# Optimization experiments

Measured on AMD Instinct MI355X. Metric: run time of the kernel, lower is better.

Reference implementation:

```python
import jax, jax.numpy as jnp
import numpy as np

N = 100_000          # nodes
E = 1_600_000        # edges (avg degree 16)
LRELU = 0.01         # default nn.LeakyReLU slope (MLP / bottleneck)
SLOPE = 0.2          # GAT attention slope


def leaky(x, s):
    return jnp.where(x >= 0, x, s * x)


def dense_block(x, convW, gamma, beta):
    # x: [N, C0]; convW: [L, G, Cmax]; each layer: BN -> LeakyReLU -> 1x1 conv -> concat
    for i in range(convW.shape[0]):
        c = x.shape[1]                       # static under trace
        mu = x.mean(axis=0)
        var = x.var(axis=0)                  # biased var, matches torch BN train mode
        xn = (x - mu) * jax.lax.rsqrt(var + 1e-5) * gamma[i, :c] + beta[i, :c]
        xn = leaky(xn, LRELU)
        x = jnp.concatenate([x, xn @ convW[i, :, :c].T], axis=1)  # [N, c+G]
    return x


def gat(x, W, a, b, src, dst):
    # single effective head (torch code shares weight/a across heads -> identical heads)
    h = x @ W                                # [N, F]
    F = W.shape[1]
    # per-edge logit: LeakyReLU([h_dst || h_src] @ a)
    e = leaky(h[dst] @ a[:F] + h[src] @ a[F:], SLOPE)   # [E]
    m = jax.ops.segment_max(e, dst, num_segments=N)
    m = jnp.where(jnp.isfinite(m), m, 0.0)
    ex = jnp.exp(e - m[dst])
    den = jax.ops.segment_sum(ex, dst, num_segments=N)
    alpha = ex / (den[dst] + 1e-16)
    out = jax.ops.segment_sum(alpha[:, None] * h[src], dst, num_segments=N)
    return out + b


def setup_inputs() -> dict:
    key = jax.random.key(0)
    ks = jax.random.split(key, 16)

    def w(k, shape, fan_in):
        return jax.random.normal(k, shape, jnp.float32) / np.float32(np.sqrt(fan_in))

    return {
        "x": jax.random.normal(ks[0], (N, 64), jnp.float32),
        "src": jax.random.randint(ks[1], (E,), 0, N, jnp.int64 if jax.config.jax_enable_x64 else jnp.int32),
        "dst": jax.random.randint(ks[2], (E,), 0, N, jnp.int64 if jax.config.jax_enable_x64 else jnp.int32),
        "mlp_w1": w(ks[3], (64, 256), 64),
        "mlp_b1": jnp.zeros((256,), jnp.float32),
        "mlp_w2": w(ks[4], (256, 256), 256),
        "mlp_b2": jnp.zeros((256,), jnp.float32),
        "mlp_w3": w(ks[5], (256, 24), 256),
        "mlp_b3": jnp.zeros((24,), jnp.float32),
        "conv1": w(ks[6], (6, 12, 84), 84),
        "bn1_g": jnp.ones((6, 84), jnp.float32),
        "bn1_b": jnp.zeros((6, 84), jnp.float32),
        "gat1_w": w(ks[7], (96, 48), 96),
        "gat1_a": jax.random.normal(ks[8], (96,), jnp.float32) * 0.1,
        "gat1_b": jnp.zeros((48,), jnp.float32),
        "conv2": w(ks[9], (6, 12, 108), 108),
        "bn2_g": jnp.ones((6, 108), jnp.float32),
        "bn2_b": jnp.zeros((6, 108), jnp.float32),
        "gat2_w": w(ks[10], (120, 60), 120),
        "gat2_a": jax.random.normal(ks[11], (120,), jnp.float32) * 0.1,
        "gat2_b": jnp.zeros((60,), jnp.float32),
        "conv3": w(ks[12], (6, 12, 120), 120),
        "bn3_g": jnp.ones((6, 120), jnp.float32),
        "bn3_b": jnp.zeros((6, 120), jnp.float32),
    }


def reference(x, src, dst,
              mlp_w1, mlp_b1, mlp_w2, mlp_b2, mlp_w3, mlp_b3,
              conv1, bn1_g, bn1_b, gat1_w, gat1_a, gat1_b,
              conv2, bn2_g, bn2_b, gat2_w, gat2_a, gat2_b,
              conv3, bn3_g, bn3_b):
    h = leaky(x @ mlp_w1 + mlp_b1, LRELU)
    h = leaky(h @ mlp_w2 + mlp_b2, LRELU)
    h = leaky(h @ mlp_w3 + mlp_b3, LRELU)          # [N, 24]
    h = dense_block(h, conv1, bn1_g, bn1_b)        # [N, 96]
    h = gat(h, gat1_w, gat1_a, gat1_b, src, dst)   # [N, 48]
    h = dense_block(h, conv2, bn2_g, bn2_b)        # [N, 120]
    h = gat(h, gat2_w, gat2_a, gat2_b, src, dst)   # [N, 60]
    h = dense_block(h, conv3, bn3_g, bn3_b)        # [N, 132]
    return h
```

## Files before the change

kernel.cpp:

```cpp
#include <hip/hip_runtime.h>
#include <math.h>

#define N_NODES 100000
#define N_EDGES 1600000

static constexpr int GG = (N_NODES + 63) / 64;
static constexpr int NB = (N_NODES + 255) / 256;
static constexpr int NBKT = (N_NODES + 255) / 256;

typedef __attribute__((ext_vector_type(8))) short          bf16x8;
typedef __attribute__((ext_vector_type(8))) unsigned short ushort8_t;
typedef __attribute__((ext_vector_type(4))) unsigned short ushort4_t;
typedef __attribute__((ext_vector_type(4))) float          f32x4;

__device__ __forceinline__ float lrelu(float v, float s){ return v >= 0.f ? v : v*s; }

__device__ __forceinline__ unsigned short f2bf(float f){
    unsigned u = __float_as_uint(f);
    unsigned r = (u + 0x7FFFu + ((u >> 16) & 1u)) >> 16;
    return (unsigned short)r;
}
__device__ __forceinline__ float bf2f(unsigned short h){
    return __uint_as_float(((unsigned)h) << 16);
}

__global__ void cvt_wT_split(const float* __restrict__ w,
                             unsigned short* __restrict__ whi,
                             unsigned short* __restrict__ wlo,
                             int K, int Nsrc, int Npad)
{
    int idx = blockIdx.x * 256 + threadIdx.x;
    if (idx >= Npad * K) return;
    int n = idx / K, k = idx % K;
    float v = (n < Nsrc) ? w[(long)k * Nsrc + n] : 0.f;
    unsigned short hi = f2bf(v);
    whi[idx] = hi;
    wlo[idx] = f2bf(v - bf2f(hi));
}

template<int KV>
__global__ __launch_bounds__(256) void mlp_mfma_hilo(
    const float* __restrict__ A,
    const unsigned short* __restrict__ wth, const unsigned short* __restrict__ wtl,
    const float* __restrict__ bias, float* __restrict__ Out)
{
    constexpr int AS = KV + 8;
    __shared__ unsigned short lds_hi[64 * AS];
    __shared__ unsigned short lds_lo[64 * AS];
    const int t = threadIdx.x;
    const int r0 = blockIdx.x * 64;
    const int wv = t >> 6, lane = t & 63;
    const int l15 = lane & 15, grp = lane >> 4;
    const int cw = wv * 64;

    constexpr int cpr = KV / 8;
    for (int c = t; c < 64 * cpr; c += 256) {
        int row = c / cpr, kc = c % cpr;
        int gr = r0 + row;
        float4 v0 = make_float4(0,0,0,0), v1 = v0;
        if (gr < N_NODES) {
            v0 = *(const float4*)(A + (long)gr * KV + kc * 8);
            v1 = *(const float4*)(A + (long)gr * KV + kc * 8 + 4);
        }
        float vs[8] = {v0.x,v0.y,v0.z,v0.w,v1.x,v1.y,v1.z,v1.w};
        unsigned short* ph = lds_hi + row * AS + kc * 8;
        unsigned short* pl = lds_lo + row * AS + kc * 8;
#pragma unroll
        for (int j = 0; j < 8; j++) {
            unsigned short hi = f2bf(vs[j]);
            ph[j] = hi;
            pl[j] = f2bf(vs[j] - bf2f(hi));
        }
    }
    __syncthreads();

    f32x4 acc[4][4];
#pragma unroll
    for (int i = 0; i < 4; i++)
#pragma unroll
        for (int j = 0; j < 4; j++) acc[i][j] = (f32x4){0.f,0.f,0.f,0.f};

#pragma unroll
    for (int ks = 0; ks < KV / 32; ks++) {
        bf16x8 ah[4], al[4], bh[4], bl[4];
#pragma unroll
        for (int i = 0; i < 4; i++) {
            ah[i] = *(const bf16x8*)(lds_hi + (i*16 + l15) * AS + ks*32 + grp*8);
            al[i] = *(const bf16x8*)(lds_lo + (i*16 + l15) * AS + ks*32 + grp*8);
        }
#pragma unroll
        for (int j = 0; j < 4; j++) {
            bh[j] = *(const bf16x8*)(wth + (size_t)(cw + j*16 + l15) * KV + ks*32 + grp*8);
            bl[j] = *(const bf16x8*)(wtl + (size_t)(cw + j*16 + l15) * KV + ks*32 + grp*8);
        }
#pragma unroll
        for (int i = 0; i < 4; i++)
#pragma unroll
            for (int j = 0; j < 4; j++) {
                acc[i][j] = __builtin_amdgcn_mfma_f32_16x16x32_bf16(ah[i], bl[j], acc[i][j], 0, 0, 0);
                acc[i][j] = __builtin_amdgcn_mfma_f32_16x16x32_bf16(al[i], bh[j], acc[i][j], 0, 0, 0);
                acc[i][j] = __builtin_amdgcn_mfma_f32_16x16x32_bf16(ah[i], bh[j], acc[i][j], 0, 0, 0);
            }
    }

    __syncthreads();
#pragma unroll
    for (int i = 0; i < 4; i++)
#pragma unroll
        for (int j = 0; j < 4; j++)
#pragma unroll
            for (int r = 0; r < 4; r++) {
                int row = r0 + i*16 + grp*4 + r;
                int col = cw + j*16 + l15;
                if (row < N_NODES) {
                    float v = acc[i][j][r] + bias[col];
                    Out[(long)row * 256 + col] = lrelu(v, 0.01f);
                }
            }
}

__global__ __launch_bounds__(256) void mlp_mfma24_hilo(
    const float* __restrict__ A,
    const unsigned short* __restrict__ wth, const unsigned short* __restrict__ wtl,
    const float* __restrict__ bias, float* __restrict__ XtOut)
{
    constexpr int KV = 256, AS = 264;
    __shared__ unsigned short lds_hi[64 * AS];
    __shared__ unsigned short lds_lo[64 * AS];
    const int t = threadIdx.x;
    const int r0 = blockIdx.x * 64;
    const int wv = t >> 6, lane = t & 63;
    const int l15 = lane & 15, grp = lane >> 4;

    constexpr int cpr = KV / 8;
    for (int c = t; c < 64 * cpr; c += 256) {
        int row = c / cpr, kc = c % cpr;
        int gr = r0 + row;
        float4 v0 = make_float4(0,0,0,0), v1 = v0;
        if (gr < N_NODES) {
            v0 = *(const float4*)(A + (long)gr * KV + kc * 8);
            v1 = *(const float4*)(A + (long)gr * KV + kc * 8 + 4);
        }
        float vs[8] = {v0.x,v0.y,v0.z,v0.w,v1.x,v1.y,v1.z,v1.w};
        unsigned short* ph = lds_hi + row * AS + kc * 8;
        unsigned short* pl = lds_lo + row * AS + kc * 8;
#pragma unroll
        for (int j = 0; j < 8; j++) {
            unsigned short hi = f2bf(vs[j]);
            ph[j] = hi;
            pl[j] = f2bf(vs[j] - bf2f(hi));
        }
    }
    __syncthreads();

    f32x4 acc[2] = {(f32x4){0.f,0.f,0.f,0.f}, (f32x4){0.f,0.f,0.f,0.f}};
#pragma unroll
    for (int ks = 0; ks < KV / 32; ks++) {
        bf16x8 ah = *(const bf16x8*)(lds_hi + (wv*16 + l15) * AS + ks*32 + grp*8);
        bf16x8 al = *(const bf16x8*)(lds_lo + (wv*16 + l15) * AS + ks*32 + grp*8);
#pragma unroll
        for (int j = 0; j < 2; j++) {
            bf16x8 bh = *(const bf16x8*)(wth + (size_t)(j*16 + l15) * KV + ks*32 + grp*8);
            bf16x8 bl = *(const bf16x8*)(wtl + (size_t)(j*16 + l15) * KV + ks*32 + grp*8);
            acc[j] = __builtin_amdgcn_mfma_f32_16x16x32_bf16(ah, bl, acc[j], 0, 0, 0);
            acc[j] = __builtin_amdgcn_mfma_f32_16x16x32_bf16(al, bh, acc[j], 0, 0, 0);
            acc[j] = __builtin_amdgcn_mfma_f32_16x16x32_bf16(ah, bh, acc[j], 0, 0, 0);
        }
    }

    __syncthreads();
    float* ldsf = (float*)lds_hi;
#pragma unroll
    for (int j = 0; j < 2; j++)
#pragma unroll
        for (int r = 0; r < 4; r++) {
            int cl = j*16 + l15;
            if (cl < 24) {
                int rl = wv*16 + grp*4 + r;
                float v = acc[j][r] + bias[cl];
                ldsf[rl * 25 + cl] = lrelu(v, 0.01f);
            }
        }
    __syncthreads();
    int n = t & 63, c0 = t >> 6;
    int gr = r0 + n;
    if (gr < N_NODES)
        for (int c = c0; c < 24; c += 4)
            XtOut[(long)c * N_NODES + gr] = ldsf[n * 25 + c];
}

__global__ void bn_stats_t(const float* __restrict__ Xt,
                           float* __restrict__ gsum, float* __restrict__ gsq)
{
    int ch = blockIdx.x, part = blockIdx.y, t = threadIdx.x;
    const float* p = Xt + (long)ch * N_NODES;
    float s = 0.f, q = 0.f;
    for (long i = (long)part * 25000 + t * 4; i < (long)(part + 1) * 25000; i += 1024) {
        float4 v = *(const float4*)(p + i);
        s += v.x + v.y + v.z + v.w;
        q += v.x*v.x + v.y*v.y + v.z*v.z + v.w*v.w;
    }
#pragma unroll
    for (int m = 1; m < 64; m <<= 1) {
        s += __shfl_xor(s, m, 64);
        q += __shfl_xor(q, m, 64);
    }
    __shared__ float ls[4], lq[4];
    int wid = t >> 6;
    if ((t & 63) == 0) { ls[wid] = s; lq[wid] = q; }
    __syncthreads();
    if (t == 0) {
        atomicAdd(gsum + ch, ls[0] + ls[1] + ls[2] + ls[3]);
        atomicAdd(gsq  + ch, lq[0] + lq[1] + lq[2] + lq[3]);
    }
}

__global__ __launch_bounds__(256) void dense_conv2(
    float* __restrict__ Xt, int C, int C0, int layerIdx,
    const float* __restrict__ W, int WS,
    const float* __restrict__ gamma, const float* __restrict__ beta,
    const float* __restrict__ gsum, const float* __restrict__ gsq,
    float* __restrict__ psq)
{
    constexpr int QOFF = 6 * 12 * NB;
    __shared__ float w_lds[12 * 132];
    __shared__ float a_lds[132], b_lds[132];
    __shared__ float red[2][4][12];
    const int t = threadIdx.x;
    const int wid = t >> 6, lane = t & 63;

    for (int c = t; c < C0; c += 256) {
        float s = gsum[c], q = gsq[c];
        float mu  = s * (1.f / N_NODES);
        float var = q * (1.f / N_NODES) - mu * mu;
        float A = rsqrtf(var + 1e-5f) * gamma[c];
        a_lds[c] = A;
        b_lds[c] = beta[c] - mu * A;
    }
    for (int gc = wid; gc < C - C0; gc += 4) {
        const float* pp = psq + (size_t)gc * NB;
        const float* qq = psq + QOFF + (size_t)gc * NB;
        float s = 0.f, q = 0.f;
        for (int b = lane; b < NB; b += 64) { s += pp[b]; q += qq[b]; }
#pragma unroll
        for (int o = 1; o < 64; o <<= 1) {
            s += __shfl_xor(s, o, 64);
            q += __shfl_xor(q, o, 64);
        }
        if (lane == 0) {
            int c = C0 + gc;
            float mu  = s * (1.f / N_NODES);
            float var = q * (1.f / N_NODES) - mu * mu;
            float A = rsqrtf(var + 1e-5f) * gamma[c];
            a_lds[c] = A;
            b_lds[c] = beta[c] - mu * A;
        }
    }
    for (int i = t; i < 12 * C; i += 256) {
        int g = i / C, c = i - g * C;
        w_lds[g * 132 + c] = W[g * WS + c];
    }
    __syncthreads();

    long n = (long)blockIdx.x * 256 + t;
    bool valid = (n < N_NODES);
    const float* xp = Xt + (valid ? n : 0);
    float acc[12];
#pragma unroll
    for (int g = 0; g < 12; g++) acc[g] = 0.f;

    float v[12], vn[12];
#pragma unroll
    for (int j = 0; j < 12; j++) v[j] = xp[(long)j * N_NODES];
    for (int c0 = 0; c0 < C; c0 += 12) {
        if (c0 + 12 < C) {
#pragma unroll
            for (int j = 0; j < 12; j++)
                vn[j] = xp[(long)(c0 + 12 + j) * N_NODES];
        }
#pragma unroll
        for (int j = 0; j < 12; j++) {
            int ch = c0 + j;
            float u = a_lds[ch] * v[j] + b_lds[ch];
            u = (u >= 0.f) ? u : 0.01f * u;
#pragma unroll
            for (int g = 0; g < 12; g++)
                acc[g] += u * w_lds[g * 132 + ch];
        }
#pragma unroll
        for (int j = 0; j < 12; j++) v[j] = vn[j];
    }
    if (valid) {
#pragma unroll
        for (int g = 0; g < 12; g++)
            Xt[(long)(C + g) * N_NODES + n] = acc[g];
    }

    if (layerIdx < 5) {
        float sv[12], qv[12];
#pragma unroll
        for (int g = 0; g < 12; g++) {
            float a = valid ? acc[g] : 0.f;
            sv[g] = a; qv[g] = a * a;
        }
#pragma unroll
        for (int m = 1; m < 64; m <<= 1)
#pragma unroll
            for (int g = 0; g < 12; g++) {
                sv[g] += __shfl_xor(sv[g], m, 64);
                qv[g] += __shfl_xor(qv[g], m, 64);
            }
        if (lane == 0) {
#pragma unroll
            for (int g = 0; g < 12; g++) { red[0][wid][g] = sv[g]; red[1][wid][g] = qv[g]; }
        }
        __syncthreads();
        if (t < 12) {
            float s = red[0][0][t] + red[0][1][t] + red[0][2][t] + red[0][3][t];
            float q = red[1][0][t] + red[1][1][t] + red[1][2][t] + red[1][3][t];
            psq[((size_t)layerIdx * 12 + t) * NB + blockIdx.x] = s;
            psq[QOFF + ((size_t)layerIdx * 12 + t) * NB + blockIdx.x] = q;
        }
    }
}

template<int F>
__global__ __launch_bounds__(256) void gat_gemm(
    const float* __restrict__ A, const float* __restrict__ B,
    const float* __restrict__ avec, int K,
    unsigned short* __restrict__ Hb, float* __restrict__ sd, float* __restrict__ ss)
{
    __shared__ float At[16 * 68];
    __shared__ float Bt[16 * 64];
    __shared__ float ad[64], as_[64];
    const int t  = threadIdx.x;
    const int r0 = blockIdx.x * 64;
    const int tx = t & 15, ty = t >> 4;
    if (t < 64) {
        ad[t]  = (t < F) ? avec[t]     : 0.f;
        as_[t] = (t < F) ? avec[F + t] : 0.f;
    }

    float acc[4][4];
#pragma unroll
    for (int i = 0; i < 4; i++)
#pragma unroll
        for (int j = 0; j < 4; j++) acc[i][j] = 0.f;

    for (int k0 = 0; k0 < K; k0 += 16) {
        {
            int kk = t >> 4, rq = t & 15;
            float4 v = make_float4(0.f,0.f,0.f,0.f);
            if (k0 + kk < K)
                v = *(const float4*)(A + (long)(k0 + kk) * N_NODES + r0 + rq * 4);
            *(float4*)(At + kk * 68 + rq * 4) = v;
        }
        for (int i = t; i < 16 * 64; i += 256) {
            int kk = i >> 6, mq = i & 63;
            float v = 0.f;
            if (k0 + kk < K && mq < F) v = B[(long)(k0 + kk) * F + mq];
            Bt[kk * 64 + mq] = v;
        }
        __syncthreads();
#pragma unroll
        for (int kk = 0; kk < 16; kk++) {
            float4 av = *(const float4*)(At + kk * 68 + ty * 4);
            float4 bv = *(const float4*)(Bt + kk * 64 + tx * 4);
            float a_[4] = {av.x, av.y, av.z, av.w};
            float b_[4] = {bv.x, bv.y, bv.z, bv.w};
#pragma unroll
            for (int i = 0; i < 4; i++)
#pragma unroll
                for (int j = 0; j < 4; j++)
                    acc[i][j] += a_[i] * b_[j];
        }
        __syncthreads();
    }

#pragma unroll
    for (int i = 0; i < 4; i++) {
        int row = r0 + ty * 4 + i;
        float pd = 0.f, pq_ = 0.f;
#pragma unroll
        for (int j = 0; j < 4; j++) {
            int col = tx * 4 + j;
            pd  += acc[i][j] * ad[col];
            pq_ += acc[i][j] * as_[col];
        }
#pragma unroll
        for (int m = 1; m < 16; m <<= 1) {
            pd  += __shfl_xor(pd,  m, 64);
            pq_ += __shfl_xor(pq_, m, 64);
        }
        if (row < N_NODES) {
            if (tx == 0) { sd[row] = pd; ss[row] = pq_; }
            if (tx * 4 < F) {
                ushort4_t u;
#pragma unroll
                for (int j = 0; j < 4; j++) u[j] = f2bf(acc[i][j]);
                *(ushort4_t*)(Hb + (long)row * 64 + tx * 4) = u;
            }
        }
    }
}

template<int F>
__global__ __launch_bounds__(256) void gat_aggregate2(
    const int* __restrict__ rstart, const int* __restrict__ csr_src,
    const float* __restrict__ sd, const float* __restrict__ ss,
    const unsigned short* __restrict__ Hb,
    const float* __restrict__ bias, float* __restrict__ outT)
{
    __shared__ float tile[64 * (F + 1)];
    const int t = threadIdx.x;
    const int wid = t >> 6, lane = t & 63;
    const long n0 = (long)blockIdx.x * 64;

#pragma unroll 1
    for (int k = 0; k < 16; k++) {
        long node = n0 + wid * 16 + k;
        float res = 0.f;
        if (node < N_NODES) {
            int st = rstart[node], en = rstart[node + 1];
            int deg = en - st;
            float sdn = sd[node];
            float acc = 0.f, dsum = 0.f;
            if (deg <= 64) {
                int sj = 0; float v = -3.4e38f;
                if (lane < deg) {
                    sj = csr_src[st + lane];
                    v = lrelu(sdn + ss[sj], 0.2f);
                }
                float m = v;
#pragma unroll
                for (int o = 1; o < 64; o <<= 1) m = fmaxf(m, __shfl_xor(m, o, 64));
                float p = (lane < deg) ? __expf(v - m) : 0.f;
                dsum = p;
                int j = 0;
                for (; j + 4 <= deg; j += 4) {
                    float a0 = __shfl(p, j, 64),   a1 = __shfl(p, j+1, 64);
                    float a2 = __shfl(p, j+2, 64), a3 = __shfl(p, j+3, 64);
                    int   s0 = __shfl(sj, j, 64),   s1 = __shfl(sj, j+1, 64);
                    int   s2 = __shfl(sj, j+2, 64), s3 = __shfl(sj, j+3, 64);
                    if (lane < F) {
                        float h0 = bf2f(Hb[(long)s0 * 64 + lane]);
                        float h1 = bf2f(Hb[(long)s1 * 64 + lane]);
                        float h2 = bf2f(Hb[(long)s2 * 64 + lane]);
                        float h3 = bf2f(Hb[(long)s3 * 64 + lane]);
                        acc += a0 * h0; acc += a1 * h1; acc += a2 * h2; acc += a3 * h3;
                    }
                }
                for (; j < deg; j++) {
                    float a = __shfl(p, j, 64);
                    int   s = __shfl(sj, j, 64);
                    if (lane < F) acc += a * bf2f(Hb[(long)s * 64 + lane]);
                }
            } else {
                float m = -3.4e38f;
                for (int base = st; base < en; base += 64) {
                    int cnt = min(64, en - base);
                    float v = -3.4e38f;
                    if (lane < cnt) {
                        int s = csr_src[base + lane];
                        v = lrelu(sdn + ss[s], 0.2f);
                    }
#pragma unroll
                    for (int o = 1; o < 64; o <<= 1) v = fmaxf(v, __shfl_xor(v, o, 64));
                    m = fmaxf(m, v);
                }
                for (int base = st; base < en; base += 64) {
                    int cnt = min(64, en - base);
                    float p = 0.f; int sj = 0;
                    if (lane < cnt) {
                        sj = csr_src[base + lane];
                        float v = lrelu(sdn + ss[sj], 0.2f);
                        p = __expf(v - m);
                    }
                    dsum += p;
                    int j = 0;
                    for (; j + 4 <= cnt; j += 4) {
                        float a0 = __shfl(p, j, 64),   a1 = __shfl(p, j+1, 64);
                        float a2 = __shfl(p, j+2, 64), a3 = __shfl(p, j+3, 64);
                        int   s0 = __shfl(sj, j, 64),   s1 = __shfl(sj, j+1, 64);
                        int   s2 = __shfl(sj, j+2, 64), s3 = __shfl(sj, j+3, 64);
                        if (lane < F) {
                            float h0 = bf2f(Hb[(long)s0 * 64 + lane]);
                            float h1 = bf2f(Hb[(long)s1 * 64 + lane]);
                            float h2 = bf2f(Hb[(long)s2 * 64 + lane]);
                            float h3 = bf2f(Hb[(long)s3 * 64 + lane]);
                            acc += a0 * h0; acc += a1 * h1; acc += a2 * h2; acc += a3 * h3;
                        }
                    }
                    for (; j < cnt; j++) {
                        float a = __shfl(p, j, 64);
                        int   s = __shfl(sj, j, 64);
                        if (lane < F) acc += a * bf2f(Hb[(long)s * 64 + lane]);
                    }
                }
            }
#pragma unroll
            for (int o = 1; o < 64; o <<= 1) dsum += __shfl_xor(dsum, o, 64);
            res = acc / (dsum + 1e-16f);
        }
        if (lane < F) tile[(wid * 16 + k) * (F + 1) + lane] = res + bias[lane];
    }
    __syncthreads();
    for (int idx = t; idx < F * 64; idx += 256) {
        int c = idx / 64, i = idx % 64;
        long n = n0 + i;
        if (n < N_NODES) outT[(long)c * N_NODES + n] = tile[i * (F + 1) + c];
    }
}

__global__ __launch_bounds__(256) void transpose_out(const float* __restrict__ Xt,
                                                     float* __restrict__ out)
{
    __shared__ float tile[64 * 133];
    int t = threadIdx.x;
    long n0 = (long)blockIdx.x * 64;
    int lane = t & 63, cq = t >> 6;
    for (int c = cq; c < 132; c += 4) {
        long n = n0 + lane;
        float v = (n < N_NODES) ? Xt[(long)c * N_NODES + n] : 0.f;
        tile[lane * 133 + c] = v;
    }
    __syncthreads();
    for (int idx = t; idx < 64 * 132; idx += 256) {
        int r = idx / 132, c = idx % 132;
        long n = n0 + r;
        if (n < N_NODES) out[n * 132 + c] = tile[r * 133 + c];
    }
}

__global__ __launch_bounds__(256) void bkt_hist(const int* __restrict__ dst,
                                                int* __restrict__ bcnt)
{
    __shared__ int lh[NBKT];
    for (int i = threadIdx.x; i < NBKT; i += 256) lh[i] = 0;
    __syncthreads();
    for (long e = (long)blockIdx.x * 256 + threadIdx.x; e < N_EDGES; e += (long)gridDim.x * 256)
        atomicAdd(&lh[dst[e] >> 8], 1);
    __syncthreads();
    for (int i = threadIdx.x; i < NBKT; i += 256)
        if (lh[i]) atomicAdd(&bcnt[i * 16], lh[i]);
}

__global__ void bkt_scan(const int* __restrict__ bcnt, int* __restrict__ boff,
                         int* __restrict__ bcur, int* __restrict__ rstart)
{
    __shared__ int ls[512];
    int t = threadIdx.x;
    int v = (t < NBKT) ? bcnt[t * 16] : 0;
    ls[t] = v; __syncthreads();
    for (int o = 1; o < 512; o <<= 1) {
        int y = (t >= o) ? ls[t - o] : 0;
        __syncthreads();
        ls[t] += y;
        __syncthreads();
    }
    if (t < NBKT) { int ex = ls[t] - v; boff[t] = ex; bcur[t * 16] = ex; }
    if (t == 0) { boff[NBKT] = N_EDGES; rstart[N_NODES] = N_EDGES; }
}

__global__ void bkt_scatter(const int* __restrict__ src, const int* __restrict__ dst,
                            int* __restrict__ bcur, int2* __restrict__ pairs)
{
    for (long e = (long)blockIdx.x * 256 + threadIdx.x; e < N_EDGES; e += (long)gridDim.x * 256) {
        int d = dst[e];
        int pos = atomicAdd(&bcur[(d >> 8) * 16], 1);
        pairs[pos] = make_int2(d, src[e]);
    }
}

__global__ __launch_bounds__(256) void bkt_build(const int2* __restrict__ pairs,
                                                 const int* __restrict__ boff,
                                                 int* __restrict__ rstart,
                                                 int* __restrict__ csr_src)
{
    __shared__ int lh[256], sc[256], lbase[256], lcur[256];
    int b = blockIdx.x, t = threadIdx.x;
    int st = boff[b], en = boff[b + 1];
    lh[t] = 0;
    __syncthreads();
    for (int i = st + t; i < en; i += 256)
        atomicAdd(&lh[pairs[i].x & 255], 1);
    __syncthreads();
    int v = lh[t];
    sc[t] = v; __syncthreads();
    for (int o = 1; o < 256; o <<= 1) {
        int y = (t >= o) ? sc[t - o] : 0;
        __syncthreads();
        sc[t] += y;
        __syncthreads();
    }
    int ex = sc[t] - v;
    lbase[t] = st + ex;
    lcur[t] = 0;
    int node = (b << 8) + t;
    if (node < N_NODES) rstart[node] = st + ex;
    __syncthreads();
    for (int i = st + t; i < en; i += 256) {
        int2 p = pairs[i];
        int ld = p.x & 255;
        int pos = lbase[ld] + atomicAdd(&lcur[ld], 1);
        csr_src[pos] = p.y;
    }
}

static void run_dense_block_t(hipStream_t stream, float* Xt, int C0,
                              const float* convW, int WS,
                              const float* gamma, const float* beta,
                              float* gsum, float* gsq, float* psq)
{
    hipMemsetAsync(gsum, 0, 264 * sizeof(float), stream);
    bn_stats_t<<<dim3(C0, 4), 256, 0, stream>>>(Xt, gsum, gsq);
    for (int i = 0; i < 6; i++) {
        int C = C0 + 12 * i;
        dense_conv2<<<NB, 256, 0, stream>>>(Xt, C, C0, i, convW + (size_t)i * 12 * WS, WS,
                                            gamma + (size_t)i * WS, beta + (size_t)i * WS,
                                            gsum, gsq, psq);
    }
}

template<int F>
static void run_gat(hipStream_t stream, const float* XtIn, int K,
                    const float* W, const float* avec, const float* bias,
                    unsigned short* Hb, float* outT,
                    float* sd, float* ss, const int* rstart, const int* csr_src)
{
    gat_gemm<F><<<GG, 256, 0, stream>>>(XtIn, W, avec, K, Hb, sd, ss);
    gat_aggregate2<F><<<GG, 256, 0, stream>>>(rstart, csr_src, sd, ss, Hb, bias, outT);
}

extern "C" void kernel_launch(void* const* d_in, const int* in_sizes, int n_in,
                              void* d_out, int out_size, void* d_ws, size_t ws_size,
                              hipStream_t stream)
{
    const float* x     = (const float*)d_in[0];
    const int*   src   = (const int*)d_in[1];
    const int*   dst   = (const int*)d_in[2];
    const float* w1    = (const float*)d_in[3];
    const float* b1    = (const float*)d_in[4];
    const float* w2    = (const float*)d_in[5];
    const float* b2    = (const float*)d_in[6];
    const float* w3    = (const float*)d_in[7];
    const float* b3    = (const float*)d_in[8];
    const float* conv1 = (const float*)d_in[9];
    const float* bn1g  = (const float*)d_in[10];
    const float* bn1b  = (const float*)d_in[11];
    const float* g1w   = (const float*)d_in[12];
    const float* g1a   = (const float*)d_in[13];
    const float* g1b   = (const float*)d_in[14];
    const float* conv2 = (const float*)d_in[15];
    const float* bn2g  = (const float*)d_in[16];
    const float* bn2b  = (const float*)d_in[17];
    const float* g2w   = (const float*)d_in[18];
    const float* g2a   = (const float*)d_in[19];
    const float* g2b   = (const float*)d_in[20];
    const float* conv3 = (const float*)d_in[21];
    const float* bn3g  = (const float*)d_in[22];
    const float* bn3b  = (const float*)d_in[23];
    float* out = (float*)d_out;

    char* ws = (char*)d_ws;
    size_t off = 0;
    auto alloc = [&](size_t bytes) -> void* {
        void* p = ws + off;
        off += (bytes + 255) & ~(size_t)255;
        return p;
    };
    float*    h      = (float*)alloc((size_t)N_NODES * 256 * 4);
    float*    Xt1    = (float*)alloc((size_t)96  * N_NODES * 4);
    float*    Xt2    = (float*)alloc((size_t)120 * N_NODES * 4);
    int*      csr_src= (int*)alloc((size_t)N_EDGES * 4);
    int2*     pairs  = (int2*)alloc((size_t)N_EDGES * 8);
    int*      rstart = (int*)alloc((size_t)(N_NODES + 1) * 4);
    int*      bcnt   = (int*)alloc((size_t)NBKT * 16 * 4);
    int*      bcur   = (int*)alloc((size_t)NBKT * 16 * 4);
    int*      boff   = (int*)alloc((size_t)(NBKT + 1) * 4);
    float*    sd     = (float*)alloc((size_t)N_NODES * 4);
    float*    ss     = (float*)alloc((size_t)N_NODES * 4);
    float*    gsum   = (float*)alloc(264 * 4);
    float*    gsq    = gsum + 132;
    float*    psq    = (float*)alloc((size_t)2 * 6 * 12 * NB * 4);
    unsigned short* wt1h = (unsigned short*)alloc(256 * 64  * 2);
    unsigned short* wt1l = (unsigned short*)alloc(256 * 64  * 2);
    unsigned short* wt2h = (unsigned short*)alloc(256 * 256 * 2);
    unsigned short* wt2l = (unsigned short*)alloc(256 * 256 * 2);
    unsigned short* wt3h = (unsigned short*)alloc(32  * 256 * 2);
    unsigned short* wt3l = (unsigned short*)alloc(32  * 256 * 2);

    unsigned short* Hb  = (unsigned short*)h;
    float* Xt3 = (float*)((char*)h + (size_t)16 * 1024 * 1024);

    hipMemsetAsync(bcnt, 0, (size_t)NBKT * 16 * 4, stream);
    bkt_hist<<<512, 256, 0, stream>>>(dst, bcnt);
    bkt_scan<<<1, 512, 0, stream>>>(bcnt, boff, bcur, rstart);
    bkt_scatter<<<2048, 256, 0, stream>>>(src, dst, bcur, pairs);
    bkt_build<<<NBKT, 256, 0, stream>>>(pairs, boff, rstart, csr_src);

    cvt_wT_split<<<(256 * 64  + 255) / 256, 256, 0, stream>>>(w1, wt1h, wt1l, 64,  256, 256);
    cvt_wT_split<<<(256 * 256 + 255) / 256, 256, 0, stream>>>(w2, wt2h, wt2l, 256, 256, 256);
    cvt_wT_split<<<(32  * 256 + 255) / 256, 256, 0, stream>>>(w3, wt3h, wt3l, 256, 24,  32);

    mlp_mfma_hilo<64> <<<GG, 256, 0, stream>>>(x, wt1h, wt1l, b1, h);
    mlp_mfma_hilo<256><<<GG, 256, 0, stream>>>(h, wt2h, wt2l, b2, h);
    mlp_mfma24_hilo<<<GG, 256, 0, stream>>>(h, wt3h, wt3l, b3, Xt1);

    run_dense_block_t(stream, Xt1, 24, conv1, 84, bn1g, bn1b, gsum, gsq, psq);

    run_gat<48>(stream, Xt1, 96, g1w, g1a, g1b, Hb, Xt2, sd, ss, rstart, csr_src);

    run_dense_block_t(stream, Xt2, 48, conv2, 108, bn2g, bn2b, gsum, gsq, psq);

    run_gat<60>(stream, Xt2, 120, g2w, g2a, g2b, Hb, Xt3, sd, ss, rstart, csr_src);

    run_dense_block_t(stream, Xt3, 60, conv3, 120, bn3g, bn3b, gsum, gsq, psq);

    transpose_out<<<GG, 256, 0, stream>>>(Xt3, out);
}
```

Measured before the change: 1.190 ms.

## Fuse three MLP layers into one kernel with packed hi/lo LDS tiles

Replaces the three separate MLP GEMM kernels with one kernel that keeps each 64-row tile's activations in shared memory across all three layers. Activations are stored packed as hi/lo bf16 pairs in 32-bit words and unpacked on read. This removes the global-memory round trips of the [N,256] intermediates and two launches. The cost is extra unpacking ALU work and a long kernel with high LDS usage.

```diff
diff --git a/kernel.cpp b/kernel.cpp
--- a/kernel.cpp
+++ b/kernel.cpp
@@ -12,6 +12,7 @@
 typedef __attribute__((ext_vector_type(8))) unsigned short ushort8_t;
 typedef __attribute__((ext_vector_type(4))) unsigned short ushort4_t;
 typedef __attribute__((ext_vector_type(4))) float          f32x4;
+typedef __attribute__((ext_vector_type(4))) unsigned       uint4v;
 
 __device__ __forceinline__ float lrelu(float v, float s){ return v >= 0.f ? v : v*s; }
 
@@ -22,6 +23,21 @@
 }
 __device__ __forceinline__ float bf2f(unsigned short h){
     return __uint_as_float(((unsigned)h) << 16);
+}
+__device__ __forceinline__ unsigned packhl(float f){
+    unsigned short hi = f2bf(f);
+    unsigned short lo = f2bf(f - bf2f(hi));
+    return (unsigned)hi | ((unsigned)lo << 16);
+}
+__device__ __forceinline__ void unpack8(const unsigned* q, bf16x8& ah, bf16x8& al){
+    unsigned a32[4], l32[4];
+#pragma unroll
+    for (int k = 0; k < 4; k++) {
+        a32[k] = (q[2*k] & 0xffffu) | (q[2*k+1] << 16);
+        l32[k] = (q[2*k] >> 16)     | (q[2*k+1] & 0xffff0000u);
+    }
+    ah = *(const bf16x8*)a32;
+    al = *(const bf16x8*)l32;
 }
 
 __global__ void cvt_wT_split(const float* __restrict__ w,
@@ -38,60 +54,60 @@
     wlo[idx] = f2bf(v - bf2f(hi));
 }
 
-template<int KV>
-__global__ __launch_bounds__(256) void mlp_mfma_hilo(
-    const float* __restrict__ A,
-    const unsigned short* __restrict__ wth, const unsigned short* __restrict__ wtl,
-    const float* __restrict__ bias, float* __restrict__ Out)
-{
-    constexpr int AS = KV + 8;
-    __shared__ unsigned short lds_hi[64 * AS];
-    __shared__ unsigned short lds_lo[64 * AS];
+__global__ __launch_bounds__(256) void mlp_fused(
+    const float* __restrict__ x,
+    const unsigned short* __restrict__ w1h, const unsigned short* __restrict__ w1l,
+    const float* __restrict__ b1,
+    const unsigned short* __restrict__ w2h, const unsigned short* __restrict__ w2l,
+    const float* __restrict__ b2,
+    const unsigned short* __restrict__ w3h, const unsigned short* __restrict__ w3l,
+    const float* __restrict__ b3,
+    float* __restrict__ XtOut)
+{
+    constexpr int AS = 260;
+    __shared__ unsigned h_pk[64 * AS];
     const int t = threadIdx.x;
     const int r0 = blockIdx.x * 64;
     const int wv = t >> 6, lane = t & 63;
     const int l15 = lane & 15, grp = lane >> 4;
     const int cw = wv * 64;
 
-    constexpr int cpr = KV / 8;
-    for (int c = t; c < 64 * cpr; c += 256) {
-        int row = c / cpr, kc = c % cpr;
-        int gr = r0 + row;
-        float4 v0 = make_float4(0,0,0,0), v1 = v0;
-        if (gr < N_NODES) {
-            v0 = *(const float4*)(A + (long)gr * KV + kc * 8);
-            v1 = *(const float4*)(A + (long)gr * KV + kc * 8 + 4);
-        }
-        float vs[8] = {v0.x,v0.y,v0.z,v0.w,v1.x,v1.y,v1.z,v1.w};
-        unsigned short* ph = lds_hi + row * AS + kc * 8;
-        unsigned short* pl = lds_lo + row * AS + kc * 8;
-#pragma unroll
-        for (int j = 0; j < 8; j++) {
-            unsigned short hi = f2bf(vs[j]);
-            ph[j] = hi;
-            pl[j] = f2bf(vs[j] - bf2f(hi));
+    {
+        int c = t;
+#pragma unroll
+        for (int it = 0; it < 4; it++, c += 256) {
+            int row = c >> 4, kq = c & 15;
+            int gr = r0 + row;
+            float4 v = make_float4(0.f, 0.f, 0.f, 0.f);
+            if (gr < N_NODES) v = *(const float4*)(x + (long)gr * 64 + kq * 4);
+            unsigned p[4] = {packhl(v.x), packhl(v.y), packhl(v.z), packhl(v.w)};
+            *(uint4v*)(h_pk + row * AS + kq * 4) = *(const uint4v*)p;
         }
     }
     __syncthreads();
 
     f32x4 acc[4][4];
+
 #pragma unroll
     for (int i = 0; i < 4; i++)
 #pragma unroll
         for (int j = 0; j < 4; j++) acc[i][j] = (f32x4){0.f,0.f,0.f,0.f};
-
-#pragma unroll
-    for (int ks = 0; ks < KV / 32; ks++) {
+#pragma unroll
+    for (int ks = 0; ks < 2; ks++) {
         bf16x8 ah[4], al[4], bh[4], bl[4];
 #pragma unroll
         for (int i = 0; i < 4; i++) {
-            ah[i] = *(const bf16x8*)(lds_hi + (i*16 + l15) * AS + ks*32 + grp*8);
-            al[i] = *(const bf16x8*)(lds_lo + (i*16 + l15) * AS + ks*32 + grp*8);
+            unsigned q[8];
+            const unsigned* p = h_pk + (i*16 + l15) * AS + ks*32 + grp*8;
+            *(uint4v*)q     = *(const uint4v*)p;
+            *(uint4v*)(q+4) = *(const uint4v*)(p + 4);
+            unpack8(q, ah[i], al[i]);
         }
 #pragma unroll
         for (int j = 0; j < 4; j++) {
-            bh[j] = *(const bf16x8*)(wth + (size_t)(cw + j*16 + l15) * KV + ks*32 + grp*8);
-            bl[j] = *(const bf16x8*)(wtl + (size_t)(cw + j*16 + l15) * KV + ks*32 + grp*8);
+            const size_t bo = (size_t)(cw + j*16 + l15) * 64 + ks*32 + grp*8;
+            bh[j] = *(const bf16x8*)(w1h + bo);
+            bl[j] = *(const bf16x8*)(w1l + bo);
         }
 #pragma unroll
         for (int i = 0; i < 4; i++)
@@ -102,74 +118,87 @@
                 acc[i][j] = __builtin_amdgcn_mfma_f32_16x16x32_bf16(ah[i], bh[j], acc[i][j], 0, 0, 0);
             }
     }
-
     __syncthreads();
 #pragma unroll
     for (int i = 0; i < 4; i++)
 #pragma unroll
-        for (int j = 0; j < 4; j++)
+        for (int j = 0; j < 4; j++) {
+            int col = cw + j*16 + l15;
+            float bv = b1[col];
 #pragma unroll
             for (int r = 0; r < 4; r++) {
-                int row = r0 + i*16 + grp*4 + r;
-                int col = cw + j*16 + l15;
-                if (row < N_NODES) {
-                    float v = acc[i][j][r] + bias[col];
-                    Out[(long)row * 256 + col] = lrelu(v, 0.01f);
-                }
+                int row = i*16 + grp*4 + r;
+                h_pk[row * AS + col] = packhl(lrelu(acc[i][j][r] + bv, 0.01f));
             }
-}
-
-__global__ __launch_bounds__(256) void mlp_mfma24_hilo(
-    const float* __restrict__ A,
-    const unsigned short* __restrict__ wth, const unsigned short* __restrict__ wtl,
-    const float* __restrict__ bias, float* __restrict__ XtOut)
-{
-    constexpr int KV = 256, AS = 264;
-    __shared__ unsigned short lds_hi[64 * AS];
-    __shared__ unsigned short lds_lo[64 * AS];
-    const int t = threadIdx.x;
-    const int r0 = blockIdx.x * 64;
-    const int wv = t >> 6, lane = t & 63;
-    const int l15 = lane & 15, grp = lane >> 4;
-
-    constexpr int cpr = KV / 8;
-    for (int c = t; c < 64 * cpr; c += 256) {
-        int row = c / cpr, kc = c % cpr;
-        int gr = r0 + row;
-        float4 v0 = make_float4(0,0,0,0), v1 = v0;
-        if (gr < N_NODES) {
-            v0 = *(const float4*)(A + (long)gr * KV + kc * 8);
-            v1 = *(const float4*)(A + (long)gr * KV + kc * 8 + 4);
-        }
-        float vs[8] = {v0.x,v0.y,v0.z,v0.w,v1.x,v1.y,v1.z,v1.w};
-        unsigned short* ph = lds_hi + row * AS + kc * 8;
-        unsigned short* pl = lds_lo + row * AS + kc * 8;
-#pragma unroll
-        for (int j = 0; j < 8; j++) {
-            unsigned short hi = f2bf(vs[j]);
-            ph[j] = hi;
-            pl[j] = f2bf(vs[j] - bf2f(hi));
-        }
-    }
-    __syncthreads();
-
-    f32x4 acc[2] = {(f32x4){0.f,0.f,0.f,0.f}, (f32x4){0.f,0.f,0.f,0.f}};
-#pragma unroll
-    for (int ks = 0; ks < KV / 32; ks++) {
-        bf16x8 ah = *(const bf16x8*)(lds_hi + (wv*16 + l15) * AS + ks*32 + grp*8);
-        bf16x8 al = *(const bf16x8*)(lds_lo + (wv*16 + l15) * AS + ks*32 + grp*8);
+        }
+    __syncthreads();
+
+#pragma unroll
+    for (int i = 0; i < 4; i++)
+#pragma unroll
+        for (int j = 0; j < 4; j++) acc[i][j] = (f32x4){0.f,0.f,0.f,0.f};
+#pragma unroll
+    for (int ks = 0; ks < 8; ks++) {
+        bf16x8 ah[4], al[4], bh[4], bl[4];
+#pragma unroll
+        for (int i = 0; i < 4; i++) {
+            unsigned q[8];
+            const unsigned* p = h_pk + (i*16 + l15) * AS + ks*32 + grp*8;
+            *(uint4v*)q     = *(const uint4v*)p;
+            *(uint4v*)(q+4) = *(const uint4v*)(p + 4);
+            unpack8(q, ah[i], al[i]);
+        }
+#pragma unroll
+        for (int j = 0; j < 4; j++) {
+            const size_t bo = (size_t)(cw + j*16 + l15) * 256 + ks*32 + grp*8;
+            bh[j] = *(const bf16x8*)(w2h + bo);
+            bl[j] = *(const bf16x8*)(w2l + bo);
+        }
+#pragma unroll
+        for (int i = 0; i < 4; i++)
+#pragma unroll
+            for (int j = 0; j < 4; j++) {
+                acc[i][j] = __builtin_amdgcn_mfma_f32_16x16x32_bf16(ah[i], bl[j], acc[i][j], 0, 0, 0);
+                acc[i][j] = __builtin_amdgcn_mfma_f32_16x16x32_bf16(al[i], bh[j], acc[i][j], 0, 0, 0);
+                acc[i][j] = __builtin_amdgcn_mfma_f32_16x16x32_bf16(ah[i], bh[j], acc[i][j], 0, 0, 0);
+            }
+    }
+    __syncthreads();
+#pragma unroll
+    for (int i = 0; i < 4; i++)
+#pragma unroll
+        for (int j = 0; j < 4; j++) {
+            int col = cw + j*16 + l15;
+            float bv = b2[col];
+#pragma unroll
+            for (int r = 0; r < 4; r++) {
+                int row = i*16 + grp*4 + r;
+                h_pk[row * AS + col] = packhl(lrelu(acc[i][j][r] + bv, 0.01f));
+            }
+        }
+    __syncthreads();
+
+    f32x4 acc3[2] = {(f32x4){0.f,0.f,0.f,0.f}, (f32x4){0.f,0.f,0.f,0.f}};
+#pragma unroll
+    for (int ks = 0; ks < 8; ks++) {
+        unsigned q[8];
+        const unsigned* p = h_pk + (wv*16 + l15) * AS + ks*32 + grp*8;
+        *(uint4v*)q     = *(const uint4v*)p;
+        *(uint4v*)(q+4) = *(const uint4v*)(p + 4);
+        bf16x8 ah, al;
+        unpack8(q, ah, al);
 #pragma unroll
         for (int j = 0; j < 2; j++) {
-            bf16x8 bh = *(const bf16x8*)(wth + (size_t)(j*16 + l15) * KV + ks*32 + grp*8);
-            bf16x8 bl = *(const bf16x8*)(wtl + (size_t)(j*16 + l15) * KV + ks*32 + grp*8);
-            acc[j] = __builtin_amdgcn_mfma_f32_16x16x32_bf16(ah, bl, acc[j], 0, 0, 0);
-            acc[j] = __builtin_amdgcn_mfma_f32_16x16x32_bf16(al, bh, acc[j], 0, 0, 0);
-            acc[j] = __builtin_amdgcn_mfma_f32_16x16x32_bf16(ah, bh, acc[j], 0, 0, 0);
-        }
-    }
-
-    __syncthreads();
-    float* ldsf = (float*)lds_hi;
+            const size_t bo = (size_t)(j*16 + l15) * 256 + ks*32 + grp*8;
+            bf16x8 bh = *(const bf16x8*)(w3h + bo);
+            bf16x8 bl = *(const bf16x8*)(w3l + bo);
+            acc3[j] = __builtin_amdgcn_mfma_f32_16x16x32_bf16(ah, bl, acc3[j], 0, 0, 0);
+            acc3[j] = __builtin_amdgcn_mfma_f32_16x16x32_bf16(al, bh, acc3[j], 0, 0, 0);
+            acc3[j] = __builtin_amdgcn_mfma_f32_16x16x32_bf16(ah, bh, acc3[j], 0, 0, 0);
+        }
+    }
+    __syncthreads();
+    float* ldsf = (float*)h_pk;
 #pragma unroll
     for (int j = 0; j < 2; j++)
 #pragma unroll
@@ -177,8 +206,7 @@
             int cl = j*16 + l15;
             if (cl < 24) {
                 int rl = wv*16 + grp*4 + r;
-                float v = acc[j][r] + bias[cl];
-                ldsf[rl * 25 + cl] = lrelu(v, 0.01f);
+                ldsf[rl * 25 + cl] = lrelu(acc3[j][r] + b3[cl], 0.01f);
             }
         }
     __syncthreads();
@@ -703,9 +731,8 @@
     cvt_wT_split<<<(256 * 256 + 255) / 256, 256, 0, stream>>>(w2, wt2h, wt2l, 256, 256, 256);
     cvt_wT_split<<<(32  * 256 + 255) / 256, 256, 0, stream>>>(w3, wt3h, wt3l, 256, 24,  32);
 
-    mlp_mfma_hilo<64> <<<GG, 256, 0, stream>>>(x, wt1h, wt1l, b1, h);
-    mlp_mfma_hilo<256><<<GG, 256, 0, stream>>>(h, wt2h, wt2l, b2, h);
-    mlp_mfma24_hilo<<<GG, 256, 0, stream>>>(h, wt3h, wt3l, b3, Xt1);
+    mlp_fused<<<GG, 256, 0, stream>>>(x, wt1h, wt1l, b1, wt2h, wt2l, b2,
+                                      wt3h, wt3l, b3, Xt1);
 
     run_dense_block_t(stream, Xt1, 24, conv1, 84, bn1g, bn1b, gsum, gsq, psq);
 
```

Measured after the change: 1.098 ms. 7.8% less time.
